# Performance work log

Measured on AMD Instinct MI355X. Metric: run time of the kernel, lower is better.

Reference implementation:

```python
import jax, jax.numpy as jnp
import numpy as np
import math

H, D = 8, 128            # num_heads, head_dim (hidden=1024)
CHUNK, PAST, FUT = 12, 12, 0
CTX = CHUNK + PAST + FUT  # 24
SOFTCAP = 50.0
INVALID = 1e-09
Q_SCALE = D ** (-0.5) / math.log(2)
K_SCALE = math.log(1.0 + math.e) / math.log(2)


def setup_inputs() -> dict:
    key = jax.random.key(0)
    ks = jax.random.split(key, 7)
    B, S, HS = 16, 2400, 1024
    w = lambda k: jax.random.normal(k, (HS, HS), jnp.float32) * 0.02
    return {
        "x": jax.random.normal(ks[0], (B, S, HS), jnp.float32),
        "pos_emb": jax.random.normal(ks[1], (CTX + 1, HS), jnp.float32),
        "Wq": w(ks[2]),
        "Wk": w(ks[3]),
        "Wv": w(ks[4]),
        "Wpost": w(ks[5]),
        "Wrel": w(ks[6]),
        "per_dim_scale": jnp.zeros((D,), jnp.float32),
    }


def _to_blocks(t):
    # [B,S,H,D] -> [B,nb,CHUNK,H,D] (pad S up to multiple of CHUNK)
    B, S, h, d = t.shape
    nb = -(-S // CHUNK)
    t = jnp.pad(t, ((0, 0), (0, nb * CHUNK - S), (0, 0), (0, 0)))
    return t.reshape(B, nb, CHUNK, h, d)


def _block_context(t):
    # [B,S,H,D] -> [B,nb,CTX,H,D]: per-block window of PAST left context + chunk + FUT
    B, S, h, d = t.shape
    nb = -(-S // CHUNK)
    tp = jnp.pad(t, ((0, 0), (PAST, FUT + CHUNK - 1), (0, 0), (0, 0)))
    idx = jnp.arange(nb)[:, None] * CHUNK + jnp.arange(CTX)[None, :]  # [nb,CTX]
    return tp[:, idx]  # gather -> [B,nb,CTX,H,D]


def _rel_shift(x):
    # [B,H,nb,CHUNK,P] -> [B,H,nb,CHUNK,CTX] via Transformer-XL reshape trick
    B, h, nb, bs, P = x.shape
    x = jnp.pad(x, ((0, 0), (0, 0), (0, 0), (0, 0), (0, CTX + 1 - P)))
    x = x.reshape(B, h, nb, bs * (CTX + 1))[..., : bs * CTX]
    return x.reshape(B, h, nb, bs, CTX)


def reference(x, pos_emb, Wq, Wk, Wv, Wpost, Wrel, per_dim_scale):
    B, S, HS = x.shape
    q = (x @ Wq).reshape(B, S, H, D) * Q_SCALE * jax.nn.softplus(per_dim_scale)
    k = (x @ Wk).reshape(B, S, H, D) * K_SCALE
    v = (x @ Wv).reshape(B, S, H, D)

    qb = _to_blocks(q)        # [B,nb,CHUNK,H,D]
    kc = _block_context(k)    # [B,nb,CTX,H,D]
    vc = _block_context(v)    # [B,nb,CTX,H,D]
    nb = qb.shape[1]

    rel_k = (pos_emb @ Wrel).reshape(-1, H, D)  # [P,H,D]

    # content-content scores: [B,H,nb,CHUNK,CTX]
    matrix_ac = jnp.einsum('bnqhd,bnkhd->bhnqk', qb, kc)
    # content-position scores with rel-shift: [B,H,nb,CHUNK,P] -> [...,CTX]
    matrix_bd = jnp.einsum('bnqhd,phd->bhnqp', qb, rel_k)
    matrix_bd = _rel_shift(matrix_bd)

    attn = jnp.tanh((matrix_ac + matrix_bd) / SOFTCAP) * SOFTCAP
    attn = jax.nn.softmax(attn, axis=-1)

    out = jnp.einsum('bhnqk,bnkhd->bnqhd', attn, vc)  # [B,nb,CHUNK,H,D]
    out = out.reshape(B, nb * CHUNK, H * D)[:, :S, :]
    return out @ Wpost
```

## Files before the change

kernel.cpp:

```cpp
#include <hip/hip_runtime.h>
#include <hip/hip_bf16.h>
#include <cmath>

#define AS_GLOBAL __attribute__((address_space(1)))
#define AS_LDS    __attribute__((address_space(3)))

typedef __attribute__((ext_vector_type(8))) short bf16x8;
typedef __attribute__((ext_vector_type(4))) float f32x4;
typedef unsigned short u16;

__device__ __forceinline__ u16 f2bf(float f) {
  union { __hip_bfloat16 h; u16 u; } cv;
  cv.h = __float2bfloat16(f);
  return cv.u;
}
__device__ __forceinline__ float bf2f(u16 u) {
  union { unsigned u32; float f; } v;
  v.u32 = ((unsigned)u) << 16;
  return v.f;
}


__global__ void k_f32_to_bf16(const float* __restrict__ in, u16* __restrict__ out, int n4) {
  int i = blockIdx.x * 256 + threadIdx.x;
  if (i >= n4) return;
  float4 v = ((const float4*)in)[i];
  ushort4 o;
  o.x = f2bf(v.x); o.y = f2bf(v.y); o.z = f2bf(v.z); o.w = f2bf(v.w);
  ((ushort4*)out)[i] = o;
}

__global__ void k_transpose_w(const float* __restrict__ in, u16* __restrict__ out) {
  __shared__ float tile[32][33];
  const int tx = threadIdx.x & 31;
  const int ty = threadIdx.x >> 5;
  const int x0 = blockIdx.x * 32, y0 = blockIdx.y * 32;
  #pragma unroll
  for (int i = 0; i < 32; i += 8)
    tile[ty + i][tx] = in[(size_t)(y0 + ty + i) * 1024 + x0 + tx];
  __syncthreads();
  #pragma unroll
  for (int i = 0; i < 32; i += 8)
    out[(size_t)(x0 + ty + i) * 1024 + y0 + tx] = f2bf(tile[tx][ty + i]);
}

__global__ void k_qscale(const float* __restrict__ pds, float* __restrict__ qs, float qscale_c) {
  int n = blockIdx.x * 256 + threadIdx.x;
  float s = pds[n & 127];
  qs[n] = qscale_c * log1pf(expf(s));
}

__global__ void k_relk(const float* __restrict__ pos, const u16* __restrict__ wrt,
                       u16* __restrict__ relkb) {
  __shared__ float prow[1024];
  const int tid = threadIdx.x;
  const int p = blockIdx.y;
  ((float4*)prow)[tid] = ((const float4*)(pos + (size_t)p * 1024))[tid];
  __syncthreads();
  int nn = blockIdx.x * 256 + tid;
  const u16* wr = wrt + (size_t)nn * 1024;
  float acc = 0.f;
  for (int kk = 0; kk < 1024; kk += 8) {
    ushort4 u0 = *(const ushort4*)(wr + kk);
    ushort4 u1 = *(const ushort4*)(wr + kk + 4);
    acc += bf2f(u0.x) * prow[kk + 0] + bf2f(u0.y) * prow[kk + 1]
         + bf2f(u0.z) * prow[kk + 2] + bf2f(u0.w) * prow[kk + 3]
         + bf2f(u1.x) * prow[kk + 4] + bf2f(u1.y) * prow[kk + 5]
         + bf2f(u1.z) * prow[kk + 6] + bf2f(u1.w) * prow[kk + 7];
  }
  relkb[(size_t)p * 1024 + nn] = f2bf(acc);
}

template <int OUTMODE>
__global__ __launch_bounds__(256) void k_gemm_bt(
    const u16* __restrict__ A, const u16* __restrict__ Bt, void* __restrict__ Cout,
    const float* __restrict__ scale_vec, float scale_scalar, int M, int N, int K) {
  __shared__ __align__(16) u16 As[128 * 32];
  __shared__ __align__(16) u16 Bs[128 * 32];
  const int tid = threadIdx.x;
  const int wave = tid >> 6, lane = tid & 63;
  const int quad = lane >> 4, l16 = lane & 15;
  const int wm = wave >> 1, wn = wave & 1;
  const int m0 = blockIdx.y * 128, n0 = blockIdx.x * 128;

  f32x4 acc[4][4];
  #pragma unroll
  for (int i = 0; i < 4; ++i)
    #pragma unroll
    for (int j = 0; j < 4; ++j) {
      f32x4 z = {0.f, 0.f, 0.f, 0.f};
      acc[i][j] = z;
    }

  for (int k0 = 0; k0 < K; k0 += 32) {
    __syncthreads();
    #pragma unroll
    for (int i = 0; i < 2; ++i) {
      int cbase = i * 256 + wave * 64;
      int c = cbase + lane;
      const u16* ga = A + (size_t)(m0 + (c >> 2)) * K + (k0 + (c & 3) * 8);
      __builtin_amdgcn_global_load_lds((const AS_GLOBAL u16*)ga, (AS_LDS u16*)&As[cbase * 8], 16, 0, 0);
      const u16* gb = Bt + (size_t)(n0 + (c >> 2)) * K + (k0 + (c & 3) * 8);
      __builtin_amdgcn_global_load_lds((const AS_GLOBAL u16*)gb, (AS_LDS u16*)&Bs[cbase * 8], 16, 0, 0);
    }
    __syncthreads();

    bf16x8 af[4], bfr[4];
    #pragma unroll
    for (int mi = 0; mi < 4; ++mi)
      af[mi] = *(const bf16x8*)&As[(wm * 64 + mi * 16 + l16) * 32 + quad * 8];
    #pragma unroll
    for (int ni = 0; ni < 4; ++ni)
      bfr[ni] = *(const bf16x8*)&Bs[(wn * 64 + ni * 16 + l16) * 32 + quad * 8];
    #pragma unroll
    for (int mi = 0; mi < 4; ++mi)
      #pragma unroll
      for (int ni = 0; ni < 4; ++ni)
        acc[mi][ni] = __builtin_amdgcn_mfma_f32_16x16x32_bf16(af[mi], bfr[ni], acc[mi][ni], 0, 0, 0);
  }

  if (OUTMODE == 2) {
    #pragma unroll
    for (int ni = 0; ni < 4; ++ni) {
      int col = n0 + wn * 64 + ni * 16 + l16;
      #pragma unroll
      for (int mi = 0; mi < 4; ++mi) {
        int row = m0 + wm * 64 + mi * 16 + quad * 4;
        ushort4 o;
        o.x = f2bf(acc[mi][ni][0]);
        o.y = f2bf(acc[mi][ni][1]);
        o.z = f2bf(acc[mi][ni][2]);
        o.w = f2bf(acc[mi][ni][3]);
        *(ushort4*)&((u16*)Cout)[(size_t)col * M + row] = o;
      }
    }
  } else {
    #pragma unroll
    for (int ni = 0; ni < 4; ++ni) {
      int col = n0 + wn * 64 + ni * 16 + l16;
      float cs = scale_vec ? scale_vec[col] : scale_scalar;
      #pragma unroll
      for (int mi = 0; mi < 4; ++mi) {
        int row = m0 + wm * 64 + mi * 16 + quad * 4;
        #pragma unroll
        for (int r = 0; r < 4; ++r) {
          float v = acc[mi][ni][r] * cs;
          if (OUTMODE == 1)
            ((u16*)Cout)[(size_t)(row + r) * N + col] = f2bf(v);
          else
            ((float*)Cout)[(size_t)(row + r) * N + col] = v;
        }
      }
    }
  }
}

__global__ __launch_bounds__(256) void k_attn_mfma(
    const u16* __restrict__ q, const u16* __restrict__ k, const u16* __restrict__ vt,
    const u16* __restrict__ relkb, u16* __restrict__ ctx) {
  __shared__ float bdm_s[4][400];
  __shared__ u16 attnb[4][16 * 32];

  const int tid = threadIdx.x;
  const int w = tid >> 6, lane = tid & 63;
  const int l16 = lane & 15, quad = lane >> 4;
  const int id = blockIdx.x * 4 + w;
  const int b = id / 1600;
  const int rr = id % 1600;
  const int n = rr >> 3, h = rr & 7;
  const int s0 = n * 12;
  const size_t rowbase = (size_t)b * 2400;

  bf16x8 qf[4];
  {
    int sq = s0 + l16;
    if (sq > 2399) sq = 2399;
    const u16* qp = q + ((rowbase + sq) * 1024 + (size_t)h * 128 + quad * 8);
    #pragma unroll
    for (int c = 0; c < 4; ++c) qf[c] = *(const bf16x8*)(qp + 32 * c);
  }

  #pragma unroll
  for (int pt = 0; pt < 2; ++pt) {
    int p = pt * 16 + l16;
    const u16* rp = relkb + ((size_t)p * 1024 + (size_t)h * 128 + quad * 8);
    f32x4 acc = {0.f, 0.f, 0.f, 0.f};
    #pragma unroll
    for (int c = 0; c < 4; ++c)
      acc = __builtin_amdgcn_mfma_f32_16x16x32_bf16(qf[c], *(const bf16x8*)(rp + 32 * c), acc, 0, 0, 0);
    if (p < 25) {
      #pragma unroll
      for (int r = 0; r < 4; ++r)
        bdm_s[w][(quad * 4 + r) * 25 + p] = acc[r];
    }
  }
  __threadfence_block();

  float l0[4], l1[4];
  #pragma unroll
  for (int kt = 0; kt < 2; ++kt) {
    int t = kt * 16 + l16;
    int sk = s0 - 12 + t;
    bool kvalid = ((unsigned)sk < 2400u);
    int ska = kvalid ? sk : 0;
    const u16* kp = k + ((rowbase + ska) * 1024 + (size_t)h * 128 + quad * 8);
    short km = kvalid ? (short)0xFFFF : (short)0;
    bf16x8 kmv = {km, km, km, km, km, km, km, km};
    f32x4 acc = {0.f, 0.f, 0.f, 0.f};
    #pragma unroll
    for (int c = 0; c < 4; ++c) {
      bf16x8 kf = *(const bf16x8*)(kp + 32 * c);
      kf &= kmv;
      acc = __builtin_amdgcn_mfma_f32_16x16x32_bf16(qf[c], kf, acc, 0, 0, 0);
    }
    #pragma unroll
    for (int r = 0; r < 4; ++r) {
      float bd = bdm_s[w][(quad * 4 + r) * 24 + t];
      float lg = tanhf((acc[r] + bd) * (1.0f / 50.0f)) * 50.0f;
      if (kt == 1 && l16 >= 8) lg = -INFINITY;
      if (kt) l1[r] = lg; else l0[r] = lg;
    }
  }

  float at0[4], at1[4];
  #pragma unroll
  for (int r = 0; r < 4; ++r) {
    float m = fmaxf(l0[r], l1[r]);
    #pragma unroll
    for (int s = 1; s < 16; s <<= 1) m = fmaxf(m, __shfl_xor(m, s, 64));
    float e0 = __expf(l0[r] - m), e1 = __expf(l1[r] - m);
    float sum = e0 + e1;
    #pragma unroll
    for (int s = 1; s < 16; s <<= 1) sum += __shfl_xor(sum, s, 64);
    float inv = 1.0f / sum;
    at0[r] = e0 * inv;
    at1[r] = e1 * inv;
  }

  #pragma unroll
  for (int r = 0; r < 4; ++r) {
    attnb[w][(quad * 4 + r) * 32 + l16] = f2bf(at0[r]);
    attnb[w][(quad * 4 + r) * 32 + 16 + l16] = f2bf(at1[r]);
  }
  __threadfence_block();
  bf16x8 af = *(const bf16x8*)&attnb[w][l16 * 32 + quad * 8];

  int slo = s0 - 12 + quad * 8;
  bf16x8 vmsk;
  #pragma unroll
  for (int j = 0; j < 8; ++j)
    vmsk[j] = ((unsigned)(slo + j) < 2400u) ? (short)0xFFFF : (short)0;

  f32x4 oacc[8];
  #pragma unroll
  for (int dt = 0; dt < 8; ++dt) {
    int col = h * 128 + dt * 16 + l16;
    const u16* vp = vt + ((size_t)col * 38400 + (long)(rowbase + s0 - 12 + quad * 8));
    ushort4 va = *(const ushort4*)vp;
    ushort4 vb = *(const ushort4*)(vp + 4);
    bf16x8 vf = {(short)va.x, (short)va.y, (short)va.z, (short)va.w,
                 (short)vb.x, (short)vb.y, (short)vb.z, (short)vb.w};
    vf &= vmsk;
    f32x4 z = {0.f, 0.f, 0.f, 0.f};
    oacc[dt] = __builtin_amdgcn_mfma_f32_16x16x32_bf16(af, vf, z, 0, 0, 0);
  }

  if (quad < 3) {
    #pragma unroll
    for (int dt = 0; dt < 8; ++dt) {
      int col = h * 128 + dt * 16 + l16;
      #pragma unroll
      for (int r = 0; r < 4; ++r) {
        int qi = quad * 4 + r;
        ctx[(rowbase + s0 + qi) * 1024 + col] = f2bf(oacc[dt][r]);
      }
    }
  }
}


extern "C" void kernel_launch(void* const* d_in, const int* in_sizes, int n_in,
                              void* d_out, int out_size, void* d_ws, size_t ws_size,
                              hipStream_t stream) {
  const float* x       = (const float*)d_in[0];
  const float* pos_emb = (const float*)d_in[1];
  const float* Wq      = (const float*)d_in[2];
  const float* Wk      = (const float*)d_in[3];
  const float* Wv      = (const float*)d_in[4];
  const float* Wpost   = (const float*)d_in[5];
  const float* Wrel    = (const float*)d_in[6];
  const float* pds     = (const float*)d_in[7];
  float* out = (float*)d_out;

  const int M = 38400, HS = 1024;
  const size_t XE = (size_t)M * HS;

  u16* xbf = (u16*)d_ws;
  u16* qbf = xbf + XE;
  u16* kbf = qbf + XE;
  u16* vt_alloc = kbf + XE;
  u16* vt = vt_alloc + 16;
  u16* wqt = vt_alloc + XE + 64;
  u16* wkt = wqt + (size_t)HS * HS;
  u16* wvt = wkt + (size_t)HS * HS;
  u16* wrt = wvt + (size_t)HS * HS;
  u16* wpt = wrt + (size_t)HS * HS;
  u16* relkb = wpt + (size_t)HS * HS;
  float* qsc = (float*)(relkb + 32 * 1024);

  const double LN2 = 0.6931471805599453;
  const float QS = (float)((1.0 / sqrt(128.0)) / LN2);
  const float KS = (float)(log(1.0 + exp(1.0)) / LN2);

  k_f32_to_bf16<<<(int)(XE / 4 / 256), 256, 0, stream>>>(x, xbf, (int)(XE / 4));
  dim3 tg(32, 32);
  k_transpose_w<<<tg, 256, 0, stream>>>(Wq, wqt);
  k_transpose_w<<<tg, 256, 0, stream>>>(Wk, wkt);
  k_transpose_w<<<tg, 256, 0, stream>>>(Wv, wvt);
  k_transpose_w<<<tg, 256, 0, stream>>>(Wrel, wrt);
  k_transpose_w<<<tg, 256, 0, stream>>>(Wpost, wpt);
  k_qscale<<<4, 256, 0, stream>>>(pds, qsc, QS);
  k_relk<<<dim3(4, 25), 256, 0, stream>>>(pos_emb, wrt, relkb);
  dim3 gg(HS / 128, M / 128);
  k_gemm_bt<1><<<gg, 256, 0, stream>>>(xbf, wqt, qbf, qsc, 1.0f, M, HS, HS);
  k_gemm_bt<1><<<gg, 256, 0, stream>>>(xbf, wkt, kbf, nullptr, KS, M, HS, HS);
  k_gemm_bt<2><<<gg, 256, 0, stream>>>(xbf, wvt, vt, nullptr, 1.0f, M, HS, HS);
  k_attn_mfma<<<25600 / 4, 256, 0, stream>>>(qbf, kbf, vt, relkb, xbf);
  k_gemm_bt<0><<<gg, 256, 0, stream>>>(xbf, wpt, out, nullptr, 1.0f, M, HS, HS);
}
```

Baseline: 963.9 us.

## Fuse Q/K/V projections into one GEMM launch with swizzled block order

Merges the three Q, K and V projection GEMMs into a single launch over a concatenated 3072-wide weight. The transposed weights sit contiguously, and a per-column scale vector carries the q scale, the k scale and 1 for v. Blocks are remapped so that groups of 8 column tiles share an A row tile, which should improve L2 reuse of x. The five weight transposes and the qscale setup are also merged into single launches. Together these aim to cut launch overhead, fill the GPU better and re-read x less often, at the cost of branchy output routing inside the GEMM epilogue.

```diff
diff --git a/kernel.cpp b/kernel.cpp
--- a/kernel.cpp
+++ b/kernel.cpp
@@ -30,8 +30,19 @@
   ((ushort4*)out)[i] = o;
 }
 
-__global__ void k_transpose_w(const float* __restrict__ in, u16* __restrict__ out) {
+__global__ void k_transpose_w5(const float* __restrict__ s0, const float* __restrict__ s1,
+                               const float* __restrict__ s2, const float* __restrict__ s3,
+                               const float* __restrict__ s4, u16* __restrict__ dbase) {
   __shared__ float tile[32][33];
+  const float* in;
+  switch (blockIdx.z) {
+    case 0: in = s0; break;
+    case 1: in = s1; break;
+    case 2: in = s2; break;
+    case 3: in = s3; break;
+    default: in = s4; break;
+  }
+  u16* out = dbase + (size_t)blockIdx.z * 1024 * 1024;
   const int tx = threadIdx.x & 31;
   const int ty = threadIdx.x >> 5;
   const int x0 = blockIdx.x * 32, y0 = blockIdx.y * 32;
@@ -44,10 +55,14 @@
     out[(size_t)(x0 + ty + i) * 1024 + y0 + tx] = f2bf(tile[tx][ty + i]);
 }
 
-__global__ void k_qscale(const float* __restrict__ pds, float* __restrict__ qs, float qscale_c) {
+__global__ void k_qscale3(const float* __restrict__ pds, float* __restrict__ qs,
+                          float qscale_c, float ks) {
   int n = blockIdx.x * 256 + threadIdx.x;
-  float s = pds[n & 127];
-  qs[n] = qscale_c * log1pf(expf(s));
+  float v;
+  if (n < 1024) v = qscale_c * log1pf(expf(pds[n & 127]));
+  else if (n < 2048) v = ks;
+  else v = 1.0f;
+  qs[n] = v;
 }
 
 __global__ void k_relk(const float* __restrict__ pos, const u16* __restrict__ wrt,
@@ -71,17 +86,23 @@
   relkb[(size_t)p * 1024 + nn] = f2bf(acc);
 }
 
-template <int OUTMODE>
+template <int KIND>
 __global__ __launch_bounds__(256) void k_gemm_bt(
-    const u16* __restrict__ A, const u16* __restrict__ Bt, void* __restrict__ Cout,
-    const float* __restrict__ scale_vec, float scale_scalar, int M, int N, int K) {
+    const u16* __restrict__ A, const u16* __restrict__ Bt,
+    u16* __restrict__ oq, u16* __restrict__ ok, u16* __restrict__ ovt,
+    float* __restrict__ ofp, const float* __restrict__ scale_vec,
+    int M, int K, int PX) {
   __shared__ __align__(16) u16 As[128 * 32];
   __shared__ __align__(16) u16 Bs[128 * 32];
+  const int gid = blockIdx.x;
+  const int cid = gid & 7, t = gid >> 3;
+  const int xb = cid + 8 * (t % PX);
+  const int yb = t / PX;
   const int tid = threadIdx.x;
   const int wave = tid >> 6, lane = tid & 63;
   const int quad = lane >> 4, l16 = lane & 15;
   const int wm = wave >> 1, wn = wave & 1;
-  const int m0 = blockIdx.y * 128, n0 = blockIdx.x * 128;
+  const int m0 = yb * 128, n0 = xb * 128;
 
   f32x4 acc[4][4];
   #pragma unroll
@@ -119,37 +140,49 @@
         acc[mi][ni] = __builtin_amdgcn_mfma_f32_16x16x32_bf16(af[mi], bfr[ni], acc[mi][ni], 0, 0, 0);
   }
 
-  if (OUTMODE == 2) {
+  if (KIND == 0) {
+    const int region = xb >> 3;
+    if (region == 2) {
+      #pragma unroll
+      for (int ni = 0; ni < 4; ++ni) {
+        int col = n0 + wn * 64 + ni * 16 + l16 - 2048;
+        #pragma unroll
+        for (int mi = 0; mi < 4; ++mi) {
+          int row = m0 + wm * 64 + mi * 16 + quad * 4;
+          ushort4 o;
+          o.x = f2bf(acc[mi][ni][0]);
+          o.y = f2bf(acc[mi][ni][1]);
+          o.z = f2bf(acc[mi][ni][2]);
+          o.w = f2bf(acc[mi][ni][3]);
+          *(ushort4*)&ovt[(size_t)col * M + row] = o;
+        }
+      }
+    } else {
+      u16* dst = region ? ok : oq;
+      #pragma unroll
+      for (int ni = 0; ni < 4; ++ni) {
+        int col = n0 + wn * 64 + ni * 16 + l16;
+        float cs = scale_vec[col];
+        int colr = col & 1023;
+        #pragma unroll
+        for (int mi = 0; mi < 4; ++mi) {
+          int row = m0 + wm * 64 + mi * 16 + quad * 4;
+          #pragma unroll
+          for (int r = 0; r < 4; ++r)
+            dst[(size_t)(row + r) * 1024 + colr] = f2bf(acc[mi][ni][r] * cs);
+        }
+      }
+    }
+  } else {
     #pragma unroll
     for (int ni = 0; ni < 4; ++ni) {
       int col = n0 + wn * 64 + ni * 16 + l16;
-      #pragma unroll
-      for (int mi = 0; mi < 4; ++mi) {
-        int row = m0 + wm * 64 + mi * 16 + quad * 4;
-        ushort4 o;
-        o.x = f2bf(acc[mi][ni][0]);
-        o.y = f2bf(acc[mi][ni][1]);
-        o.z = f2bf(acc[mi][ni][2]);
-        o.w = f2bf(acc[mi][ni][3]);
-        *(ushort4*)&((u16*)Cout)[(size_t)col * M + row] = o;
-      }
-    }
-  } else {
-    #pragma unroll
-    for (int ni = 0; ni < 4; ++ni) {
-      int col = n0 + wn * 64 + ni * 16 + l16;
-      float cs = scale_vec ? scale_vec[col] : scale_scalar;
       #pragma unroll
       for (int mi = 0; mi < 4; ++mi) {
         int row = m0 + wm * 64 + mi * 16 + quad * 4;
         #pragma unroll
-        for (int r = 0; r < 4; ++r) {
-          float v = acc[mi][ni][r] * cs;
-          if (OUTMODE == 1)
-            ((u16*)Cout)[(size_t)(row + r) * N + col] = f2bf(v);
-          else
-            ((float*)Cout)[(size_t)(row + r) * N + col] = v;
-        }
+        for (int r = 0; r < 4; ++r)
+          ofp[(size_t)(row + r) * 1024 + col] = acc[mi][ni][r];
       }
     }
   }
@@ -313,18 +346,10 @@
   const float KS = (float)(log(1.0 + exp(1.0)) / LN2);
 
   k_f32_to_bf16<<<(int)(XE / 4 / 256), 256, 0, stream>>>(x, xbf, (int)(XE / 4));
-  dim3 tg(32, 32);
-  k_transpose_w<<<tg, 256, 0, stream>>>(Wq, wqt);
-  k_transpose_w<<<tg, 256, 0, stream>>>(Wk, wkt);
-  k_transpose_w<<<tg, 256, 0, stream>>>(Wv, wvt);
-  k_transpose_w<<<tg, 256, 0, stream>>>(Wrel, wrt);
-  k_transpose_w<<<tg, 256, 0, stream>>>(Wpost, wpt);
-  k_qscale<<<4, 256, 0, stream>>>(pds, qsc, QS);
+  k_transpose_w5<<<dim3(32, 32, 5), 256, 0, stream>>>(Wq, Wk, Wv, Wrel, Wpost, wqt);
+  k_qscale3<<<12, 256, 0, stream>>>(pds, qsc, QS, KS);
   k_relk<<<dim3(4, 25), 256, 0, stream>>>(pos_emb, wrt, relkb);
-  dim3 gg(HS / 128, M / 128);
-  k_gemm_bt<1><<<gg, 256, 0, stream>>>(xbf, wqt, qbf, qsc, 1.0f, M, HS, HS);
-  k_gemm_bt<1><<<gg, 256, 0, stream>>>(xbf, wkt, kbf, nullptr, KS, M, HS, HS);
-  k_gemm_bt<2><<<gg, 256, 0, stream>>>(xbf, wvt, vt, nullptr, 1.0f, M, HS, HS);
+  k_gemm_bt<0><<<7200, 256, 0, stream>>>(xbf, wqt, qbf, kbf, vt, nullptr, qsc, M, HS, 3);
   k_attn_mfma<<<25600 / 4, 256, 0, stream>>>(qbf, kbf, vt, relkb, xbf);
-  k_gemm_bt<0><<<gg, 256, 0, stream>>>(xbf, wpt, out, nullptr, 1.0f, M, HS, HS);
-}
+  k_gemm_bt<1><<<2400, 256, 0, stream>>>(xbf, wpt, nullptr, nullptr, nullptr, out, nullptr, M, HS, 1);
+}
```

After: 967.9 us. Within noise of the previous version (+0.4%).
